# Kernel tuning notes

Hardware: AMD Instinct MI355X
Metric: run time of the kernel (lower is better)

The kernel has to match this reference:

```python
import jax, jax.numpy as jnp
import numpy as np

DIM = 1024
NH = 16
HD = DIM // NH
EPS = 1e-5


def setup_inputs() -> dict:
    key = jax.random.key(0)
    ks = jax.random.split(key, 6)
    B, LQ, LK = 8, 512, 1024
    s = 1.0 / np.sqrt(DIM)
    return {
        "text_tokens": jax.random.normal(ks[0], (B, LQ, DIM), dtype=jnp.float32),
        "vision_tokens": jax.random.normal(ks[1], (B, LK, DIM), dtype=jnp.float32),
        "in_proj_w": jax.random.normal(ks[2], (3 * DIM, DIM), dtype=jnp.float32) * s,
        "in_proj_b": jnp.zeros((3 * DIM,), dtype=jnp.float32),
        "out_w": jax.random.normal(ks[3], (DIM, DIM), dtype=jnp.float32) * s,
        "out_b": jnp.zeros((DIM,), dtype=jnp.float32),
        "ln_g": jnp.ones((DIM,), dtype=jnp.float32),
        "ln_b": jnp.zeros((DIM,), dtype=jnp.float32),
    }


def _layernorm(x, g, b):
    mu = jnp.mean(x, axis=-1, keepdims=True)
    var = jnp.mean(jnp.square(x - mu), axis=-1, keepdims=True)
    return (x - mu) * jax.lax.rsqrt(var + EPS) * g + b


def reference(text_tokens, vision_tokens, in_proj_w, in_proj_b, out_w, out_b, ln_g, ln_b):
    B, LQ, _ = text_tokens.shape
    LK = vision_tokens.shape[1]
    wq, wk, wv = in_proj_w[:DIM], in_proj_w[DIM:2 * DIM], in_proj_w[2 * DIM:]
    bq, bk, bv = in_proj_b[:DIM], in_proj_b[DIM:2 * DIM], in_proj_b[2 * DIM:]
    q = (text_tokens @ wq.T + bq).reshape(B, LQ, NH, HD)
    k = (vision_tokens @ wk.T + bk).reshape(B, LK, NH, HD)
    v = (vision_tokens @ wv.T + bv).reshape(B, LK, NH, HD)
    scale = 1.0 / np.sqrt(HD)
    scores = jnp.einsum("bqhd,bkhd->bhqk", q, k) * scale  # [B,H,LQ,LK]
    probs = jax.nn.softmax(scores, axis=-1)
    ctx = jnp.einsum("bhqk,bkhd->bqhd", probs, v).reshape(B, LQ, DIM)
    attended = ctx @ out_w.T + out_b
    out = _layernorm(attended + text_tokens, ln_g, ln_b)
    attn_weights = jnp.mean(probs, axis=1)  # PyTorch average_attn_weights=True
    return out, attn_weights
```

## Files before the change

### kernel.cpp

```cpp
#include <hip/hip_runtime.h>

#define DIMV 1024
#define NHV  16
#define HDV  64
#define BV   8
#define LQV  512
#define LKV  1024
#define PSTR 1032

typedef __bf16 bfrag  __attribute__((ext_vector_type(8)));
typedef float  f32x4  __attribute__((ext_vector_type(4)));
typedef unsigned short u16;
typedef unsigned int   u32;
typedef unsigned long long u64;
typedef u16 u16x8 __attribute__((ext_vector_type(8)));

typedef const __attribute__((address_space(1))) u32 gu32;
typedef __attribute__((address_space(3))) u32 lu32;

__device__ __forceinline__ u16 f2bf(float f) {
    u32 x = __builtin_bit_cast(u32, f);
    x = x + 0x7FFFu + ((x >> 16) & 1u);
    return (u16)(x >> 16);
}

__device__ __forceinline__ float b2f(u16 v) {
    u32 x = ((u32)v) << 16;
    return __builtin_bit_cast(float, x);
}

__device__ __forceinline__ void g2l16(const u16* g, const u16* l) {
    __builtin_amdgcn_global_load_lds(
        reinterpret_cast<gu32*>(reinterpret_cast<u64>(g)),
        reinterpret_cast<lu32*>((u32)reinterpret_cast<u64>(l)),
        16, 0, 0);
}

__global__ __launch_bounds__(256)
void cast_all(const float* __restrict__ vis,  const float* __restrict__ wqkv,
              const float* __restrict__ outw, const float* __restrict__ text,
              u16* __restrict__ vis_bf, u16* __restrict__ wqkv_bf,
              u16* __restrict__ outw_bf, u16* __restrict__ text_bf)
{
    const int bx = blockIdx.x;
    const float* src; u16* dst; int i;
    if (bx < 8192)       { src = vis;  dst = vis_bf;  i = bx * 256 + threadIdx.x; }
    else if (bx < 11264) { src = wqkv; dst = wqkv_bf; i = (bx - 8192) * 256 + threadIdx.x; }
    else if (bx < 12288) { src = outw; dst = outw_bf; i = (bx - 11264) * 256 + threadIdx.x; }
    else                 { src = text; dst = text_bf; i = (bx - 12288) * 256 + threadIdx.x; }
    const float4 v = reinterpret_cast<const float4*>(src)[i];
    ushort4 o;
    o.x = f2bf(v.x); o.y = f2bf(v.y); o.z = f2bf(v.z); o.w = f2bf(v.w);
    reinterpret_cast<ushort4*>(dst)[i] = o;
}

__global__ __launch_bounds__(256)
void qkv_gemm(const u16* __restrict__ text_bf, const u16* __restrict__ vis_bf,
              const u16* __restrict__ wqkv_bf, const float* __restrict__ bqkv,
              u16* __restrict__ qb, u16* __restrict__ kb, u16* __restrict__ vTb)
{
    __shared__ __align__(16) u16 sA[128 * 64];
    __shared__ __align__(16) u16 sB[128 * 64];

    const int bx = blockIdx.x;
    const u16* A; const u16* W; const float* bias; u16* C; int mb, vmode;
    if (bx < 32)      { A = text_bf; W = wqkv_bf;               bias = bqkv;        C = qb;  mb = bx * 128;        vmode = 0; }
    else if (bx < 96) { A = vis_bf;  W = wqkv_bf + 1024 * 1024; bias = bqkv + 1024; C = kb;  mb = (bx - 32) * 128; vmode = 0; }
    else              { A = vis_bf;  W = wqkv_bf + 2097152;     bias = bqkv + 2048; C = vTb; mb = (bx - 96) * 128; vmode = 1; }

    const int t    = threadIdx.x;
    const int lane = t & 63;
    const int w    = t >> 6;
    const int quad = lane >> 4;
    const int r    = lane & 15;
    const int wr   = (w >> 1) * 64;
    const int wc   = (w & 1) * 64;
    const int nb   = blockIdx.y * 128;

    const int srow  = lane >> 3;
    const int skoff = (lane & 7) * 8;

    f32x4 acc[4][4] = {};

    const u16* Abase = A + (size_t)mb * 1024 + skoff;
    const u16* Wbase = W + (size_t)nb * 1024 + skoff;

    for (int k0 = 0; k0 < 1024; k0 += 64) {
#pragma unroll
        for (int it = 0; it < 4; ++it) {
            const int c = w * 4 + it;
            const int row = c * 8 + srow;
            g2l16(Abase + (size_t)row * 1024 + k0, sA + c * 512);
            g2l16(Wbase + (size_t)row * 1024 + k0, sB + c * 512);
        }
        __syncthreads();
#pragma unroll
        for (int kk = 0; kk < 2; ++kk) {
            bfrag af[4], bg[4];
#pragma unroll
            for (int i = 0; i < 4; ++i)
                af[i] = *reinterpret_cast<const bfrag*>(sA + (wr + i * 16 + r) * 64 + kk * 32 + quad * 8);
#pragma unroll
            for (int j = 0; j < 4; ++j)
                bg[j] = *reinterpret_cast<const bfrag*>(sB + (wc + j * 16 + r) * 64 + kk * 32 + quad * 8);
#pragma unroll
            for (int i = 0; i < 4; ++i)
#pragma unroll
                for (int j = 0; j < 4; ++j)
                    acc[i][j] = __builtin_amdgcn_mfma_f32_16x16x32_bf16(af[i], bg[j], acc[i][j], 0, 0, 0);
        }
        __syncthreads();
    }

#pragma unroll
    for (int i = 0; i < 4; i++)
#pragma unroll
    for (int j = 0; j < 4; j++) {
        const int colg = nb + wc + j * 16 + r;
        const float bv = bias[colg];
#pragma unroll
        for (int reg = 0; reg < 4; reg++) {
            const int rowg = mb + wr + i * 16 + quad * 4 + reg;
            const float v = acc[i][j][reg] + bv;
            if (vmode == 0) {
                C[(size_t)rowg * 1024 + colg] = f2bf(v);
            } else {
                C[((size_t)((rowg >> 10) << 10) + colg) * 1024 + (rowg & 1023)] = f2bf(v);
            }
        }
    }
}

__global__ __launch_bounds__(256)
void gemm_out(const u16* __restrict__ A, const u16* __restrict__ W,
              const float* __restrict__ bias, float* __restrict__ Cout,
              const float* __restrict__ resid)
{
    __shared__ __align__(16) u16 sA[128 * 64];
    __shared__ __align__(16) u16 sB[128 * 64];

    const int t    = threadIdx.x;
    const int lane = t & 63;
    const int w    = t >> 6;
    const int quad = lane >> 4;
    const int r    = lane & 15;
    const int wr   = (w >> 1) * 64;
    const int wc   = (w & 1) * 64;
    const int mb   = blockIdx.x * 128;
    const int nb   = blockIdx.y * 128;

    const int srow  = lane >> 3;
    const int skoff = (lane & 7) * 8;

    f32x4 acc[4][4] = {};

    const u16* Abase = A + (size_t)mb * 1024 + skoff;
    const u16* Wbase = W + (size_t)nb * 1024 + skoff;

    for (int k0 = 0; k0 < 1024; k0 += 64) {
#pragma unroll
        for (int it = 0; it < 4; ++it) {
            const int c = w * 4 + it;
            const int row = c * 8 + srow;
            g2l16(Abase + (size_t)row * 1024 + k0, sA + c * 512);
            g2l16(Wbase + (size_t)row * 1024 + k0, sB + c * 512);
        }
        __syncthreads();
#pragma unroll
        for (int kk = 0; kk < 2; ++kk) {
            bfrag af[4], bg[4];
#pragma unroll
            for (int i = 0; i < 4; ++i)
                af[i] = *reinterpret_cast<const bfrag*>(sA + (wr + i * 16 + r) * 64 + kk * 32 + quad * 8);
#pragma unroll
            for (int j = 0; j < 4; ++j)
                bg[j] = *reinterpret_cast<const bfrag*>(sB + (wc + j * 16 + r) * 64 + kk * 32 + quad * 8);
#pragma unroll
            for (int i = 0; i < 4; ++i)
#pragma unroll
                for (int j = 0; j < 4; ++j)
                    acc[i][j] = __builtin_amdgcn_mfma_f32_16x16x32_bf16(af[i], bg[j], acc[i][j], 0, 0, 0);
        }
        __syncthreads();
    }

#pragma unroll
    for (int i = 0; i < 4; i++)
#pragma unroll
    for (int j = 0; j < 4; j++) {
        const int colg = nb + wc + j * 16 + r;
        const float bv = bias[colg];
#pragma unroll
        for (int reg = 0; reg < 4; reg++) {
            const int rowg = mb + wr + i * 16 + quad * 4 + reg;
            const float v = acc[i][j][reg] + bv;
            Cout[(size_t)rowg * 1024 + colg] = v + resid[(size_t)rowg * 1024 + colg];
        }
    }
}

__global__ __launch_bounds__(512, 2)
void attn_kernel(const u16* __restrict__ q, const u16* __restrict__ k,
                 const u16* __restrict__ vT, u16* __restrict__ ctx,
                 float* __restrict__ attnw)
{
    __shared__ __align__(16) u16 sP[2][2][16 * PSTR];
    __shared__ float reds[2][2][64];

    const int t    = threadIdx.x;
    const int g    = t >> 8;
    const int tg   = t & 255;
    const int lane = tg & 63;
    const int w    = tg >> 6;
    const int quad = lane >> 4;
    const int r    = lane & 15;
    const int b    = blockIdx.x;
    const int q0   = blockIdx.y * 16;

    const int row16 = quad * 4;
    const float scale = 0.125f;

    const int arow = t & 15;
    const int ac0  = (t >> 4) * 32;

    float wacc[32] = {};

    for (int hh = 0; hh < 8; ++hh) {
        const int h = g * 8 + hh;
        const int p = hh & 1;
        const int dbase = h * HDV + quad * 8;

        const u16* qp = q + (size_t)(b * LQV + q0 + r) * DIMV + dbase;
        const bfrag qa0 = *reinterpret_cast<const bfrag*>(qp);
        const bfrag qa1 = *reinterpret_cast<const bfrag*>(qp + 32);

        float sw[4] = {0.f, 0.f, 0.f, 0.f};
#pragma unroll
        for (int ch = 0; ch < 4; ++ch) {
            f32x4 s4[4];
#pragma unroll
            for (int u = 0; u < 4; ++u) {
                const int i = ch * 4 + u;
                const u16* kp = k + (size_t)(b * LKV + w * 256 + i * 16 + r) * DIMV + dbase;
                const bfrag kb0 = *reinterpret_cast<const bfrag*>(kp);
                const bfrag kb1 = *reinterpret_cast<const bfrag*>(kp + 32);
                f32x4 a = {};
                a     = __builtin_amdgcn_mfma_f32_16x16x32_bf16(qa0, kb0, a, 0, 0, 0);
                s4[u] = __builtin_amdgcn_mfma_f32_16x16x32_bf16(qa1, kb1, a, 0, 0, 0);
            }
#pragma unroll
            for (int u = 0; u < 4; ++u) {
                const int i = ch * 4 + u;
#pragma unroll
                for (int reg = 0; reg < 4; ++reg) {
                    const float e = __expf(s4[u][reg] * scale);
                    sw[reg] += e;
                    sP[g][p][(row16 + reg) * PSTR + w * 256 + i * 16 + r] = f2bf(e);
                }
            }
        }

#pragma unroll
        for (int reg = 0; reg < 4; ++reg)
#pragma unroll
            for (int off = 1; off < 16; off <<= 1)
                sw[reg] += __shfl_xor(sw[reg], off);
        if (r == 0) {
#pragma unroll
            for (int reg = 0; reg < 4; ++reg)
                reds[g][p][w * 16 + row16 + reg] = sw[reg];
        }

        __syncthreads();

        float factor[4];
#pragma unroll
        for (int reg = 0; reg < 4; ++reg) {
            const int rr = row16 + reg;
            factor[reg] = 1.0f / (reds[g][p][rr]      + reds[g][p][16 + rr] +
                                  reds[g][p][32 + rr] + reds[g][p][48 + rr]);
        }

        {
            const float f0 = 1.0f / (reds[0][p][arow]      + reds[0][p][16 + arow] +
                                     reds[0][p][32 + arow] + reds[0][p][48 + arow]);
            const float f1 = 1.0f / (reds[1][p][arow]      + reds[1][p][16 + arow] +
                                     reds[1][p][32 + arow] + reds[1][p][48 + arow]);
#pragma unroll
            for (int m = 0; m < 4; ++m) {
                const u16x8 p0 = *reinterpret_cast<const u16x8*>(&sP[0][p][arow * PSTR + ac0 + m * 8]);
                const u16x8 p1 = *reinterpret_cast<const u16x8*>(&sP[1][p][arow * PSTR + ac0 + m * 8]);
#pragma unroll
                for (int e = 0; e < 8; ++e)
                    wacc[m * 8 + e] += b2f(p0[e]) * f0 + b2f(p1[e]) * f1;
            }
        }

        {
            const int n0 = w * 16;
            f32x4 c0 = {}, c1 = {}, c2 = {}, c3 = {};
            const u16* vb = vT + (size_t)(b * DIMV + h * HDV + n0 + r) * LKV;
            const u16* sPb = &sP[g][p][r * PSTR + quad * 8];
            __builtin_amdgcn_s_setprio(1);
#pragma unroll
            for (int kk = 0; kk < LKV; kk += 128) {
                const bfrag a0 = *reinterpret_cast<const bfrag*>(sPb + kk);
                const bfrag a1 = *reinterpret_cast<const bfrag*>(sPb + kk + 32);
                const bfrag a2 = *reinterpret_cast<const bfrag*>(sPb + kk + 64);
                const bfrag a3 = *reinterpret_cast<const bfrag*>(sPb + kk + 96);
                const bfrag b0 = *reinterpret_cast<const bfrag*>(vb + kk      + quad * 8);
                const bfrag b1 = *reinterpret_cast<const bfrag*>(vb + kk + 32 + quad * 8);
                const bfrag b2 = *reinterpret_cast<const bfrag*>(vb + kk + 64 + quad * 8);
                const bfrag b3 = *reinterpret_cast<const bfrag*>(vb + kk + 96 + quad * 8);
                c0 = __builtin_amdgcn_mfma_f32_16x16x32_bf16(a0, b0, c0, 0, 0, 0);
                c1 = __builtin_amdgcn_mfma_f32_16x16x32_bf16(a1, b1, c1, 0, 0, 0);
                c2 = __builtin_amdgcn_mfma_f32_16x16x32_bf16(a2, b2, c2, 0, 0, 0);
                c3 = __builtin_amdgcn_mfma_f32_16x16x32_bf16(a3, b3, c3, 0, 0, 0);
            }
            __builtin_amdgcn_s_setprio(0);
            const f32x4 c = (c0 + c1) + (c2 + c3);
#pragma unroll
            for (int reg = 0; reg < 4; ++reg)
                ctx[(size_t)(b * LQV + q0 + row16 + reg) * DIMV + h * HDV + n0 + r] =
                    f2bf(c[reg] * factor[reg]);
        }
    }

    {
        const float inv16 = 1.0f / 16.0f;
        float* ap = attnw + (size_t)(b * LQV + q0 + arow) * LKV + ac0;
#pragma unroll
        for (int j = 0; j < 32; j += 4) {
            float4 o;
            o.x = wacc[j]     * inv16;
            o.y = wacc[j + 1] * inv16;
            o.z = wacc[j + 2] * inv16;
            o.w = wacc[j + 3] * inv16;
            *reinterpret_cast<float4*>(ap + j) = o;
        }
    }
}

__global__ __launch_bounds__(256)
void ln_kernel(const float* __restrict__ x, const float* __restrict__ g,
               const float* __restrict__ bta, float* __restrict__ out)
{
    __shared__ float red[8];
    const int row = blockIdx.x;
    const int t = threadIdx.x;
    const int w = t >> 6;
    const float4 xv = reinterpret_cast<const float4*>(x + (size_t)row * DIMV)[t];

    float s = xv.x + xv.y + xv.z + xv.w;
#pragma unroll
    for (int off = 32; off; off >>= 1) s += __shfl_down(s, off);
    if ((t & 63) == 0) red[w] = s;
    __syncthreads();
    const float mu = (red[0] + red[1] + red[2] + red[3]) * (1.0f / 1024.0f);

    const float d0 = xv.x - mu, d1 = xv.y - mu, d2 = xv.z - mu, d3 = xv.w - mu;
    float s2 = d0 * d0 + d1 * d1 + d2 * d2 + d3 * d3;
#pragma unroll
    for (int off = 32; off; off >>= 1) s2 += __shfl_down(s2, off);
    if ((t & 63) == 0) red[4 + w] = s2;
    __syncthreads();
    const float var = (red[4] + red[5] + red[6] + red[7]) * (1.0f / 1024.0f);
    const float inv = rsqrtf(var + 1e-5f);

    float4 o;
    const int c = t * 4;
    o.x = d0 * inv * g[c + 0] + bta[c + 0];
    o.y = d1 * inv * g[c + 1] + bta[c + 1];
    o.z = d2 * inv * g[c + 2] + bta[c + 2];
    o.w = d3 * inv * g[c + 3] + bta[c + 3];
    reinterpret_cast<float4*>(out + (size_t)row * DIMV)[t] = o;
}

extern "C" void kernel_launch(void* const* d_in, const int* in_sizes, int n_in,
                              void* d_out, int out_size, void* d_ws, size_t ws_size,
                              hipStream_t stream)
{
    const float* text = (const float*)d_in[0];
    const float* vis  = (const float*)d_in[1];
    const float* wqkv = (const float*)d_in[2];
    const float* bqkv = (const float*)d_in[3];
    const float* outw = (const float*)d_in[4];
    const float* outb = (const float*)d_in[5];
    const float* lng  = (const float*)d_in[6];
    const float* lnb  = (const float*)d_in[7];

    char* ws = (char*)d_ws;
    u16*   vis_bf  = (u16*)(ws);
    u16*   ctxb    = (u16*)(ws);
    u16*   wqkv_bf = (u16*)(ws + (size_t)(16u << 20));
    u16*   outw_bf = (u16*)(ws + (size_t)(22u << 20));
    u16*   qb      = (u16*)(ws + (size_t)(24u << 20));
    u16*   kb      = (u16*)(ws + (size_t)(32u << 20));
    float* attb    = (float*)(ws + (size_t)(32u << 20));
    u16*   vTb     = (u16*)(ws + (size_t)(48u << 20));

    float* outp  = (float*)d_out;
    float* attnw = outp + (size_t)4096 * 1024;
    u16*   text_bf = (u16*)outp;

    const dim3 blk(256);
    cast_all<<<dim3(16384), blk, 0, stream>>>(vis, wqkv, outw, text,
                                              vis_bf, wqkv_bf, outw_bf, text_bf);
    qkv_gemm<<<dim3(160, 8), blk, 0, stream>>>(text_bf, vis_bf, wqkv_bf, bqkv, qb, kb, vTb);
    attn_kernel<<<dim3(8, 32), dim3(512), 0, stream>>>(qb, kb, vTb, ctxb, attnw);
    gemm_out<<<dim3(32, 8), blk, 0, stream>>>(ctxb, outw_bf, outb, attb, text);
    ln_kernel<<<dim3(4096), blk, 0, stream>>>(attb, lng, lnb, outp);
}
```

Before: 377.1 us.

## Split-K the output GEMM and widen attention blocks to four head groups

The output projection GEMM is split along K into two halves that write separate partial buffers. The LayerNorm kernel then sums both partials with the residual and bias, so the GEMM grid grows from 256 to 512 blocks and fills more CUs. The attention kernel moves to 1024 threads with four head groups of four heads each instead of two groups of eight. It drops the double-buffered P scratch and adds a barrier after each head. The cost is extra partial-sum memory traffic, one extra barrier per head, and lower occupancy per CU for attention.

```diff
diff --git a/kernel.cpp b/kernel.cpp
--- a/kernel.cpp
+++ b/kernel.cpp
@@ -133,8 +133,7 @@
 
 __global__ __launch_bounds__(256)
 void gemm_out(const u16* __restrict__ A, const u16* __restrict__ W,
-              const float* __restrict__ bias, float* __restrict__ Cout,
-              const float* __restrict__ resid)
+              float* __restrict__ attb)
 {
     __shared__ __align__(16) u16 sA[128 * 64];
     __shared__ __align__(16) u16 sB[128 * 64];
@@ -148,6 +147,8 @@
     const int wc   = (w & 1) * 64;
     const int mb   = blockIdx.x * 128;
     const int nb   = blockIdx.y * 128;
+    const int z    = blockIdx.z;
+    float* Cout    = attb + (size_t)z * 4096 * 1024;
 
     const int srow  = lane >> 3;
     const int skoff = (lane & 7) * 8;
@@ -157,7 +158,7 @@
     const u16* Abase = A + (size_t)mb * 1024 + skoff;
     const u16* Wbase = W + (size_t)nb * 1024 + skoff;
 
-    for (int k0 = 0; k0 < 1024; k0 += 64) {
+    for (int k0 = z * 512; k0 < z * 512 + 512; k0 += 64) {
 #pragma unroll
         for (int it = 0; it < 4; ++it) {
             const int c = w * 4 + it;
@@ -189,23 +190,21 @@
 #pragma unroll
     for (int j = 0; j < 4; j++) {
         const int colg = nb + wc + j * 16 + r;
-        const float bv = bias[colg];
 #pragma unroll
         for (int reg = 0; reg < 4; reg++) {
             const int rowg = mb + wr + i * 16 + quad * 4 + reg;
-            const float v = acc[i][j][reg] + bv;
-            Cout[(size_t)rowg * 1024 + colg] = v + resid[(size_t)rowg * 1024 + colg];
-        }
-    }
-}
-
-__global__ __launch_bounds__(512, 2)
+            Cout[(size_t)rowg * 1024 + colg] = acc[i][j][reg];
+        }
+    }
+}
+
+__global__ __launch_bounds__(1024)
 void attn_kernel(const u16* __restrict__ q, const u16* __restrict__ k,
                  const u16* __restrict__ vT, u16* __restrict__ ctx,
                  float* __restrict__ attnw)
 {
-    __shared__ __align__(16) u16 sP[2][2][16 * PSTR];
-    __shared__ float reds[2][2][64];
+    __shared__ __align__(16) u16 sP[4][16 * PSTR];
+    __shared__ float reds[4][64];
 
     const int t    = threadIdx.x;
     const int g    = t >> 8;
@@ -221,13 +220,12 @@
     const float scale = 0.125f;
 
     const int arow = t & 15;
-    const int ac0  = (t >> 4) * 32;
-
-    float wacc[32] = {};
-
-    for (int hh = 0; hh < 8; ++hh) {
-        const int h = g * 8 + hh;
-        const int p = hh & 1;
+    const int ac0  = (t >> 4) * 16;
+
+    float wacc[16] = {};
+
+    for (int hh = 0; hh < 4; ++hh) {
+        const int h = g * 4 + hh;
         const int dbase = h * HDV + quad * 8;
 
         const u16* qp = q + (size_t)(b * LQV + q0 + r) * DIMV + dbase;
@@ -255,7 +253,7 @@
                 for (int reg = 0; reg < 4; ++reg) {
                     const float e = __expf(s4[u][reg] * scale);
                     sw[reg] += e;
-                    sP[g][p][(row16 + reg) * PSTR + w * 256 + i * 16 + r] = f2bf(e);
+                    sP[g][(row16 + reg) * PSTR + w * 256 + i * 16 + r] = f2bf(e);
                 }
             }
         }
@@ -268,7 +266,7 @@
         if (r == 0) {
 #pragma unroll
             for (int reg = 0; reg < 4; ++reg)
-                reds[g][p][w * 16 + row16 + reg] = sw[reg];
+                reds[g][w * 16 + row16 + reg] = sw[reg];
         }
 
         __syncthreads();
@@ -277,22 +275,25 @@
 #pragma unroll
         for (int reg = 0; reg < 4; ++reg) {
             const int rr = row16 + reg;
-            factor[reg] = 1.0f / (reds[g][p][rr]      + reds[g][p][16 + rr] +
-                                  reds[g][p][32 + rr] + reds[g][p][48 + rr]);
+            factor[reg] = 1.0f / (reds[g][rr]      + reds[g][16 + rr] +
+                                  reds[g][32 + rr] + reds[g][48 + rr]);
         }
 
         {
-            const float f0 = 1.0f / (reds[0][p][arow]      + reds[0][p][16 + arow] +
-                                     reds[0][p][32 + arow] + reds[0][p][48 + arow]);
-            const float f1 = 1.0f / (reds[1][p][arow]      + reds[1][p][16 + arow] +
-                                     reds[1][p][32 + arow] + reds[1][p][48 + arow]);
-#pragma unroll
-            for (int m = 0; m < 4; ++m) {
-                const u16x8 p0 = *reinterpret_cast<const u16x8*>(&sP[0][p][arow * PSTR + ac0 + m * 8]);
-                const u16x8 p1 = *reinterpret_cast<const u16x8*>(&sP[1][p][arow * PSTR + ac0 + m * 8]);
-#pragma unroll
-                for (int e = 0; e < 8; ++e)
-                    wacc[m * 8 + e] += b2f(p0[e]) * f0 + b2f(p1[e]) * f1;
+            float fg[4];
+#pragma unroll
+            for (int gg = 0; gg < 4; ++gg)
+                fg[gg] = 1.0f / (reds[gg][arow]      + reds[gg][16 + arow] +
+                                 reds[gg][32 + arow] + reds[gg][48 + arow]);
+#pragma unroll
+            for (int gg = 0; gg < 4; ++gg) {
+                const u16x8 p0 = *reinterpret_cast<const u16x8*>(&sP[gg][arow * PSTR + ac0]);
+                const u16x8 p1 = *reinterpret_cast<const u16x8*>(&sP[gg][arow * PSTR + ac0 + 8]);
+#pragma unroll
+                for (int e = 0; e < 8; ++e) {
+                    wacc[e]     += b2f(p0[e]) * fg[gg];
+                    wacc[8 + e] += b2f(p1[e]) * fg[gg];
+                }
             }
         }
 
@@ -300,7 +301,7 @@
             const int n0 = w * 16;
             f32x4 c0 = {}, c1 = {}, c2 = {}, c3 = {};
             const u16* vb = vT + (size_t)(b * DIMV + h * HDV + n0 + r) * LKV;
-            const u16* sPb = &sP[g][p][r * PSTR + quad * 8];
+            const u16* sPb = &sP[g][r * PSTR + quad * 8];
             __builtin_amdgcn_s_setprio(1);
 #pragma unroll
             for (int kk = 0; kk < LKV; kk += 128) {
@@ -324,13 +325,15 @@
                 ctx[(size_t)(b * LQV + q0 + row16 + reg) * DIMV + h * HDV + n0 + r] =
                     f2bf(c[reg] * factor[reg]);
         }
+
+        __syncthreads();
     }
 
     {
         const float inv16 = 1.0f / 16.0f;
         float* ap = attnw + (size_t)(b * LQV + q0 + arow) * LKV + ac0;
 #pragma unroll
-        for (int j = 0; j < 32; j += 4) {
+        for (int j = 0; j < 16; j += 4) {
             float4 o;
             o.x = wacc[j]     * inv16;
             o.y = wacc[j + 1] * inv16;
@@ -342,14 +345,24 @@
 }
 
 __global__ __launch_bounds__(256)
-void ln_kernel(const float* __restrict__ x, const float* __restrict__ g,
-               const float* __restrict__ bta, float* __restrict__ out)
+void ln_kernel(const float* __restrict__ a0, const float* __restrict__ a1,
+               const float* __restrict__ resid, const float* __restrict__ ob,
+               const float* __restrict__ g, const float* __restrict__ bta,
+               float* __restrict__ out)
 {
     __shared__ float red[8];
     const int row = blockIdx.x;
     const int t = threadIdx.x;
     const int w = t >> 6;
-    const float4 xv = reinterpret_cast<const float4*>(x + (size_t)row * DIMV)[t];
+    const float4 v0 = reinterpret_cast<const float4*>(a0 + (size_t)row * DIMV)[t];
+    const float4 v1 = reinterpret_cast<const float4*>(a1 + (size_t)row * DIMV)[t];
+    const float4 vr = reinterpret_cast<const float4*>(resid + (size_t)row * DIMV)[t];
+    const float4 vb = reinterpret_cast<const float4*>(ob)[t];
+    float4 xv;
+    xv.x = v0.x + v1.x + vr.x + vb.x;
+    xv.y = v0.y + v1.y + vr.y + vb.y;
+    xv.z = v0.z + v1.z + vr.z + vb.z;
+    xv.w = v0.w + v1.w + vr.w + vb.w;
 
     float s = xv.x + xv.y + xv.z + xv.w;
 #pragma unroll
@@ -407,7 +420,8 @@
     cast_all<<<dim3(16384), blk, 0, stream>>>(vis, wqkv, outw, text,
                                               vis_bf, wqkv_bf, outw_bf, text_bf);
     qkv_gemm<<<dim3(160, 8), blk, 0, stream>>>(text_bf, vis_bf, wqkv_bf, bqkv, qb, kb, vTb);
-    attn_kernel<<<dim3(8, 32), dim3(512), 0, stream>>>(qb, kb, vTb, ctxb, attnw);
-    gemm_out<<<dim3(32, 8), blk, 0, stream>>>(ctxb, outw_bf, outb, attb, text);
-    ln_kernel<<<dim3(4096), blk, 0, stream>>>(attb, lng, lnb, outp);
-}
+    attn_kernel<<<dim3(8, 32), dim3(1024), 0, stream>>>(qb, kb, vTb, ctxb, attnw);
+    gemm_out<<<dim3(32, 8, 2), blk, 0, stream>>>(ctxb, outw_bf, attb);
+    ln_kernel<<<dim3(4096), blk, 0, stream>>>(attb, attb + (size_t)4096 * 1024,
+                                              text, outb, lng, lnb, outp);
+}
```

After: 368.7 us. 1.02x faster.
